# Kernel optimization log

Measured on AMD Instinct MI355X. Metric: run time of the kernel, lower is better.

## Reference

```python
import jax, jax.numpy as jnp
import numpy as np
import math

H = 16          # num_heads
EPS = 1e-5      # LayerNorm eps (torch default)


def setup_inputs() -> dict:
    key = jax.random.key(0)
    ks = jax.random.split(key, 4)
    B, T, D = 2, 2048, 1024
    s = 1.0 / math.sqrt(D)
    return {
        "x": jax.random.normal(ks[0], (B, T, D), dtype=jnp.float32),
        "ln_g": jnp.ones((D,), jnp.float32),
        "ln_b": jnp.zeros((D,), jnp.float32),
        "Wq": jax.random.normal(ks[1], (D, D), jnp.float32) * s,
        "bq": jnp.zeros((D,), jnp.float32),
        "Wk": jax.random.normal(ks[2], (D, D), jnp.float32) * s,
        "bk": jnp.zeros((D,), jnp.float32),
        "Wv": jax.random.normal(ks[3], (D, D), jnp.float32) * s,
        "bv": jnp.zeros((D,), jnp.float32),
    }


def reference(x, ln_g, ln_b, Wq, bq, Wk, bk, Wv, bv):
    B, T, D = x.shape
    # LayerNorm (shared across the three projections, computed once)
    mu = jnp.mean(x, axis=-1, keepdims=True)
    var = jnp.mean(jnp.square(x - mu), axis=-1, keepdims=True)
    xn = (x - mu) * jax.lax.rsqrt(var + EPS) * ln_g + ln_b
    # Q/K/V projections -> [B, T, H, Dh]
    q = (xn @ Wq + bq).reshape(B, T, H, D // H)
    k = (xn @ Wk + bk).reshape(B, T, H, D // H)
    v = (xn @ Wv + bv).reshape(B, T, H, D // H)
    # QK^T scores [B, n, m, h], scaled by sqrt(head_dim)
    scale = 1.0 / math.sqrt(D // H)
    attn = jnp.einsum('bnhd,bmhd->bnmh', q, k) * scale
    # softmax over key axis (dim=2), dropout p=0 is identity
    w = jax.nn.softmax(attn, axis=2)
    # weighted sum of values, merge heads
    y = jnp.einsum('bnmh,bmhd->bnhd', w, v).reshape(B, T, D)
    return y
```

## Files before the change

kernel.cpp:

```cpp
#include <hip/hip_runtime.h>
#include <hip/hip_bf16.h>


typedef __attribute__((ext_vector_type(8)))  short short8;
typedef __attribute__((ext_vector_type(4)))  float f32x4;
typedef __attribute__((ext_vector_type(2)))  float f32x2;
typedef __attribute__((ext_vector_type(16))) float f32x16;
typedef __attribute__((ext_vector_type(2)))  unsigned int uint2v;

#define D_MODEL 1024
#define T_SEQ   2048
#define NHEAD   16
#define HDIM    64

#define LOG2E 1.4426950408889634f

#if defined(__has_builtin)
#if __has_builtin(__builtin_amdgcn_exp2f)
#define EXP2(x) __builtin_amdgcn_exp2f(x)
#endif
#if __has_builtin(__builtin_amdgcn_permlane32_swap)
#define HAVE_PERMSWAP 1
#endif
#endif
#ifndef EXP2
#define EXP2(x) exp2f(x)
#endif

__device__ __forceinline__ unsigned short f2bf(float x) {
    unsigned int u = __float_as_uint(x);
    u = (u + 0x7fffu + ((u >> 16) & 1u)) >> 16;
    return (unsigned short)u;
}

__device__ __forceinline__ uint2v permswap(unsigned a, unsigned b) {
#ifdef HAVE_PERMSWAP
    return __builtin_amdgcn_permlane32_swap(a, b, false, false);
#else
    uint2v r;
    const unsigned as = (unsigned)__shfl_xor((int)a, 32, 64);
    const unsigned bs = (unsigned)__shfl_xor((int)b, 32, 64);
    const bool hi = (threadIdx.x & 32) != 0;
    r[0] = hi ? bs : a;
    r[1] = hi ? b  : as;
    return r;
#endif
}

__device__ __forceinline__ void w8(unsigned short* p, const uint4 v) {
    uint2 a; a.x = v.x; a.y = v.y;
    uint2 b; b.x = v.z; b.y = v.w;
    *(uint2*)p = a;
    *(uint2*)(p + 4) = b;
}

__device__ __forceinline__ short8 read8(const unsigned short* p) {
    union { unsigned u[4]; short8 s; } r;
    const uint2 a = *(const uint2*)p;
    const uint2 b = *(const uint2*)(p + 4);
    r.u[0] = a.x; r.u[1] = a.y; r.u[2] = b.x; r.u[3] = b.y;
    return r.s;
}

__global__ __launch_bounds__(256) void ln_wcast_kernel(
    const float* __restrict__ x, const float* __restrict__ gam,
    const float* __restrict__ bet, unsigned short* __restrict__ xn,
    const float* __restrict__ Wq, const float* __restrict__ Wk,
    const float* __restrict__ Wv, unsigned short* __restrict__ Wt)
{
    __shared__ float red[8];
    __shared__ float tile[32][33];
    const int bid = blockIdx.x;
    if (bid < 4096) {
        const int row = bid;
        const int t = threadIdx.x;
        const float4 v = ((const float4*)(x + (size_t)row * D_MODEL))[t];
        float s  = v.x + v.y + v.z + v.w;
        float s2 = v.x * v.x + v.y * v.y + v.z * v.z + v.w * v.w;
#pragma unroll
        for (int off = 32; off; off >>= 1) {
            s  += __shfl_down(s,  off, 64);
            s2 += __shfl_down(s2, off, 64);
        }
        const int lane = t & 63, wave = t >> 6;
        if (lane == 0) { red[wave] = s; red[4 + wave] = s2; }
        __syncthreads();
        s  = red[0] + red[1] + red[2] + red[3];
        s2 = red[4] + red[5] + red[6] + red[7];
        const float mu   = s * (1.f / D_MODEL);
        const float var  = s2 * (1.f / D_MODEL) - mu * mu;
        const float rstd = rsqrtf(var + 1e-5f);
        const float4 gv = ((const float4*)gam)[t];
        const float4 bv = ((const float4*)bet)[t];
        ushort4 o;
        o.x = f2bf((v.x - mu) * rstd * gv.x + bv.x);
        o.y = f2bf((v.y - mu) * rstd * gv.y + bv.y);
        o.z = f2bf((v.z - mu) * rstd * gv.z + bv.z);
        o.w = f2bf((v.w - mu) * rstd * gv.w + bv.w);
        ((ushort4*)(xn + (size_t)row * D_MODEL))[t] = o;
    } else {
        const int id = bid - 4096;
        const int z  = id >> 10;
        const int t2 = id & 1023;
        const int n0 = (t2 & 31) * 32, k0 = (t2 >> 5) * 32;
        const float* W = (z == 0) ? Wq : (z == 1) ? Wk : Wv;
        unsigned short* outw = Wt + (size_t)z * D_MODEL * D_MODEL;
        const int tx = threadIdx.x & 31, ty = threadIdx.x >> 5;
#pragma unroll
        for (int i = ty; i < 32; i += 8)
            tile[i][tx] = W[(size_t)(k0 + i) * D_MODEL + n0 + tx];
        __syncthreads();
#pragma unroll
        for (int i = ty; i < 32; i += 8)
            outw[(size_t)(n0 + i) * D_MODEL + k0 + tx] = f2bf(tile[tx][i]);
    }
}

__global__ __launch_bounds__(256) void qkv_gemm_kernel(
    const unsigned short* __restrict__ xn, const unsigned short* __restrict__ Wt,
    const float* __restrict__ bq, const float* __restrict__ bk, const float* __restrict__ bv,
    unsigned short* __restrict__ qo, unsigned short* __restrict__ ko, unsigned short* __restrict__ vt)
{
    const int which = blockIdx.x >> 3;
    const int xt = blockIdx.x & 7, yt = blockIdx.y;
    const bool vmode = (which == 2);
    const unsigned short* Aptr = vmode ? (Wt + (size_t)2 * D_MODEL * D_MODEL) : xn;
    const unsigned short* Bptr = vmode ? xn : (Wt + (size_t)which * D_MODEL * D_MODEL);
    const float* bias   = (which == 0) ? bq : (which == 1) ? bk : bv;
    const float scale   = (which == 0) ? (0.125f * LOG2E) : 1.0f;
    const int m0 = vmode ? (yt & 15) * 64 : yt * 64;
    const int n0 = vmode ? (xt + (yt >> 4) * 8) * 128 : xt * 128;

    __shared__ unsigned short As[64][64];
    __shared__ unsigned short Bs[128][64];

    const int tid = threadIdx.x;
    const int lane = tid & 63, wave = tid >> 6;
    const int wc = wave;
    const int g = lane >> 4, c = lane & 15;

    const int srow = lane >> 3;
    const int swzc = (((lane & 7) * 8) ^ ((srow & 7) * 8));
    const int rsw  = (c & 7) * 8;

    f32x4 acc[4][2] = {};

    for (int kt = 0; kt < D_MODEL; kt += 64) {
        __syncthreads();
#pragma unroll
        for (int i = 0; i < 2; ++i) {
            const int r = wave * 16 + i * 8;
            const unsigned short* ga = Aptr + (size_t)(m0 + r + srow) * D_MODEL + kt + swzc;
            __builtin_amdgcn_global_load_lds(
                (const __attribute__((address_space(1))) unsigned int*)ga,
                (__attribute__((address_space(3))) unsigned int*)(&As[r][0]), 16, 0, 0);
        }
#pragma unroll
        for (int i = 0; i < 4; ++i) {
            const int r = wave * 32 + i * 8;
            const unsigned short* gb = Bptr + (size_t)(n0 + r + srow) * D_MODEL + kt + swzc;
            __builtin_amdgcn_global_load_lds(
                (const __attribute__((address_space(1))) unsigned int*)gb,
                (__attribute__((address_space(3))) unsigned int*)(&Bs[r][0]), 16, 0, 0);
        }
        __syncthreads();

        short8 af[4][2], bf[2][2];
#pragma unroll
        for (int i = 0; i < 4; ++i) {
            const int ra = i * 16 + c;
#pragma unroll
            for (int kk = 0; kk < 2; ++kk)
                af[i][kk] = *(const short8*)(&As[ra][(kk * 32 + g * 8) ^ rsw]);
        }
#pragma unroll
        for (int j = 0; j < 2; ++j) {
            const int rb = wc * 32 + j * 16 + c;
#pragma unroll
            for (int kk = 0; kk < 2; ++kk)
                bf[j][kk] = *(const short8*)(&Bs[rb][(kk * 32 + g * 8) ^ rsw]);
        }
#pragma unroll
        for (int kk = 0; kk < 2; ++kk)
#pragma unroll
            for (int i = 0; i < 4; ++i)
#pragma unroll
                for (int j = 0; j < 2; ++j)
                    acc[i][j] = __builtin_amdgcn_mfma_f32_16x16x32_bf16(
                        af[i][kk], bf[j][kk], acc[i][j], 0, 0, 0);
    }

    if (!vmode) {
        unsigned short* out = (which == 0) ? qo : ko;
#pragma unroll
        for (int j = 0; j < 2; ++j) {
            const int n = n0 + wc * 32 + j * 16 + c;
            const float bn = bias[n];
            const int h = n >> 6, dh = n & 63;
#pragma unroll
            for (int i = 0; i < 4; ++i) {
#pragma unroll
                for (int r = 0; r < 4; ++r) {
                    const int m = m0 + i * 16 + g * 4 + r;
                    const int bb = m >> 11, t = m & 2047;
                    out[((size_t)(bb * NHEAD + h) * T_SEQ + t) * HDIM + dh] =
                        f2bf((acc[i][j][r] + bn) * scale);
                }
            }
        }
    } else {
#pragma unroll
        for (int i = 0; i < 4; ++i) {
#pragma unroll
            for (int r = 0; r < 4; ++r) {
                const int m = m0 + i * 16 + g * 4 + r;
                const float bn = bias[m];
#pragma unroll
                for (int j = 0; j < 2; ++j) {
                    const int n = n0 + wc * 32 + j * 16 + c;
                    const int bb = n >> 11, t = n & 2047;
                    vt[(size_t)bb * (D_MODEL * T_SEQ) + (size_t)m * T_SEQ + t] =
                        f2bf(acc[i][j][r] + bn);
                }
            }
        }
    }
}

__global__ __launch_bounds__(256, 4) void attn_kernel(
    const unsigned short* __restrict__ qb, const unsigned short* __restrict__ kb,
    const unsigned short* __restrict__ vtb, float* __restrict__ out)
{
    const int id  = blockIdx.x;
    const int swz = (id & 7) * 128 + (id >> 3);
    const int qt  = swz & 31;
    const int bh  = swz >> 5;
    const int b = bh >> 4, head = bh & 15;
    const unsigned short* Q  = qb  + (size_t)bh * T_SEQ * HDIM;
    const unsigned short* Kp = kb  + (size_t)bh * T_SEQ * HDIM;
    const unsigned short* Vt = vtb + (size_t)b * (D_MODEL * T_SEQ)
                                   + (size_t)head * (HDIM * T_SEQ);

    __shared__ __align__(16) unsigned short smem[17920];

    const int tid = threadIdx.x, lane = tid & 63, wave = tid >> 6;
    const int w2 = wave & 1, kvh = wave >> 1;
    const int q = lane & 31, h = lane >> 5;
    const int kvbase = kvh * (T_SEQ / 2);

    unsigned short* kbuf = &smem[wave * 4480];
    unsigned short* vbuf = kbuf + 2176;

    const int krow = lane >> 3, kch = (lane & 7) * 8;
    const int vrow = lane >> 2, vch = (lane & 3) * 8;

    short8 qf[4];
    {
        const unsigned short* qp = Q + (size_t)(qt * 64 + w2 * 32 + q) * HDIM;
#pragma unroll
        for (int c = 0; c < 4; ++c)
            qf[c] = *(const short8*)(qp + c * 16 + h * 8);
    }

    float l_r = 0.f;
    f32x16 o[2] = {};

    {
        const unsigned short* kp = Kp + (size_t)(kvbase + krow) * HDIM + kch;
        const unsigned short* vp = Vt + (size_t)vrow * T_SEQ + kvbase + vch;
        uint4 kr[4], vr[4];
#pragma unroll
        for (int i = 0; i < 4; ++i) kr[i] = *(const uint4*)(kp + (size_t)i * 8 * HDIM);
#pragma unroll
        for (int i = 0; i < 4; ++i) vr[i] = *(const uint4*)(vp + (size_t)i * 16 * T_SEQ);
#pragma unroll
        for (int i = 0; i < 4; ++i) w8(kbuf + (i * 8 + krow) * 68 + kch, kr[i]);
#pragma unroll
        for (int i = 0; i < 4; ++i) w8(vbuf + (i * 16 + vrow) * 36 + vch, vr[i]);
    }

#pragma unroll 1
    for (int t = 0; t < 32; ++t) {
        const bool more = (t + 1 < 32);
        const int kvn = kvbase + (t + 1) * 32;

        uint4 kr[4];
        if (more) {
            const unsigned short* kp = Kp + (size_t)(kvn + krow) * HDIM + kch;
#pragma unroll
            for (int i = 0; i < 4; ++i) kr[i] = *(const uint4*)(kp + (size_t)i * 8 * HDIM);
        }

        f32x16 s = {};
#pragma unroll
        for (int c = 0; c < 4; ++c) {
            const short8 kf = read8(kbuf + (size_t)q * 68 + c * 16 + h * 8);
            s = __builtin_amdgcn_mfma_f32_32x32x16_bf16(kf, qf[c], s, 0, 0, 0);
        }

#pragma unroll
        for (int r = 0; r < 16; ++r) { s[r] = EXP2(s[r]); }

        {
            f32x2 u[8];
#pragma unroll
            for (int r = 0; r < 8; ++r) { f32x2 a; a[0] = s[2*r]; a[1] = s[2*r+1]; u[r] = a; }
            u[0] += u[1]; u[2] += u[3]; u[4] += u[5]; u[6] += u[7];
            u[0] += u[2]; u[4] += u[6];
            u[0] += u[4];
            float rs = u[0][0] + u[0][1];
            rs += __shfl_xor(rs, 32, 64);
            l_r += rs;
        }

        unsigned Wb[8];
#pragma unroll
        for (int u = 0; u < 4; ++u) {
            asm("v_cvt_pk_bf16_f32 %0, %1, %2" : "=v"(Wb[u*2])   : "v"(s[4*u]),   "v"(s[4*u+1]));
            asm("v_cvt_pk_bf16_f32 %0, %1, %2" : "=v"(Wb[u*2+1]) : "v"(s[4*u+2]), "v"(s[4*u+3]));
        }

        short8 pf[2];
#pragma unroll
        for (int m = 0; m < 2; ++m) {
            const uint2v r0 = permswap(Wb[4*m],     Wb[4*m + 2]);
            const uint2v r1 = permswap(Wb[4*m + 1], Wb[4*m + 3]);
            union { unsigned u[4]; short8 s; } pw;
            pw.u[0] = r0[0]; pw.u[1] = r1[0]; pw.u[2] = r0[1]; pw.u[3] = r1[1];
            pf[m] = pw.s;
        }

        if (more) {
#pragma unroll
            for (int i = 0; i < 4; ++i) w8(kbuf + (i * 8 + krow) * 68 + kch, kr[i]);
        }
        uint4 vr[4];
        if (more) {
            const unsigned short* vp = Vt + (size_t)vrow * T_SEQ + kvn + vch;
#pragma unroll
            for (int i = 0; i < 4; ++i) vr[i] = *(const uint4*)(vp + (size_t)i * 16 * T_SEQ);
        }

#pragma unroll
        for (int dt = 0; dt < 2; ++dt) {
#pragma unroll
            for (int kk = 0; kk < 2; ++kk) {
                const short8 vf = read8(vbuf + (size_t)(dt * 32 + q) * 36 + kk * 16 + h * 8);
                o[dt] = __builtin_amdgcn_mfma_f32_32x32x16_bf16(vf, pf[kk], o[dt], 0, 0, 0);
            }
        }

        if (more) {
#pragma unroll
            for (int i = 0; i < 4; ++i) w8(vbuf + (i * 16 + vrow) * 36 + vch, vr[i]);
        }
    }

    __syncthreads();
    float* obuf  = (float*)(void*)smem;
    float* l_lds = ((float*)(void*)smem) + 64 * 68;

    const int qrl = w2 * 32 + q;
    if (kvh == 0) {
#pragma unroll
        for (int dt = 0; dt < 2; ++dt)
#pragma unroll
            for (int u = 0; u < 4; ++u) {
                float* dst = obuf + (size_t)qrl * 68 + dt * 32 + 8 * u + 4 * h;
                float2 lo; lo.x = o[dt][4*u];     lo.y = o[dt][4*u + 1];
                float2 hi; hi.x = o[dt][4*u + 2]; hi.y = o[dt][4*u + 3];
                *(float2*)dst = lo;
                *(float2*)(dst + 2) = hi;
            }
        if (h == 0) l_lds[qrl] = l_r;
    }
    __syncthreads();
    if (kvh == 1) {
        const float invl = 1.0f / (l_lds[qrl] + l_r);
#pragma unroll
        for (int dt = 0; dt < 2; ++dt)
#pragma unroll
            for (int u = 0; u < 4; ++u) {
                float* dst = obuf + (size_t)qrl * 68 + dt * 32 + 8 * u + 4 * h;
                float2 lo = *(const float2*)dst;
                float2 hi = *(const float2*)(dst + 2);
                lo.x = (lo.x + o[dt][4*u])     * invl;
                lo.y = (lo.y + o[dt][4*u + 1]) * invl;
                hi.x = (hi.x + o[dt][4*u + 2]) * invl;
                hi.y = (hi.y + o[dt][4*u + 3]) * invl;
                *(float2*)dst = lo;
                *(float2*)(dst + 2) = hi;
            }
    }
    __syncthreads();
#pragma unroll
    for (int it = 0; it < 2; ++it) {
        const int row = it * 32 + (tid >> 3);
        const int col = (tid & 7) * 8;
        const float4 v0 = *(const float4*)(&obuf[(size_t)row * 68 + col]);
        const float4 v1 = *(const float4*)(&obuf[(size_t)row * 68 + col + 4]);
        float* op = &out[(size_t)(b * T_SEQ + qt * 64 + row) * D_MODEL + head * HDIM + col];
        *(float4*)op = v0;
        *(float4*)(op + 4) = v1;
    }
}

extern "C" void kernel_launch(void* const* d_in, const int* in_sizes, int n_in,
                              void* d_out, int out_size, void* d_ws, size_t ws_size,
                              hipStream_t stream)
{
    const float* x   = (const float*)d_in[0];
    const float* lng = (const float*)d_in[1];
    const float* lnb = (const float*)d_in[2];
    const float* Wq  = (const float*)d_in[3];
    const float* bq  = (const float*)d_in[4];
    const float* Wk  = (const float*)d_in[5];
    const float* bk  = (const float*)d_in[6];
    const float* Wv  = (const float*)d_in[7];
    const float* bv  = (const float*)d_in[8];
    float* out = (float*)d_out;

    unsigned short* xn = (unsigned short*)d_ws;
    unsigned short* Wt = xn + (size_t)4096 * 1024;
    unsigned short* qh = Wt + (size_t)3 * 1024 * 1024;
    unsigned short* kh = qh + (size_t)4096 * 1024;
    unsigned short* vt = kh + (size_t)4096 * 1024;

    ln_wcast_kernel<<<7168, 256, 0, stream>>>(x, lng, lnb, xn, Wq, Wk, Wv, Wt);
    qkv_gemm_kernel<<<dim3(24, 64), 256, 0, stream>>>(xn, Wt, bq, bk, bv, qh, kh, vt);
    attn_kernel<<<1024, 256, 0, stream>>>(qh, kh, vt, out);
}
```

Before: 111.9 us.

## Share double-buffered K/V LDS tiles across wave pairs in attention and swizzle GEMM grid

The attention kernel now has each pair of waves that covers the same KV half load one shared K/V tile cooperatively. This halves the per-wave global loads and LDS writes. The tile is double-buffered in LDS, synchronized with a block barrier each iteration, and the MFMA sections are raised in priority with s_setprio. The V tile row pitch shrinks to 34 elements, which may break 8-byte alignment of the LDS accesses. Separately, the QKV GEMM launch becomes a 1D grid with a block swizzle for better cache locality, and the weight transpose-cast uses vectorized float4 loads and ushort4 stores.

```diff
diff --git a/kernel.cpp b/kernel.cpp
--- a/kernel.cpp
+++ b/kernel.cpp
@@ -45,6 +45,12 @@
     r[1] = hi ? b  : as;
     return r;
 #endif
+}
+
+__device__ __forceinline__ void group_barrier() {
+    asm volatile("s_waitcnt lgkmcnt(0)" ::: "memory");
+    __builtin_amdgcn_s_barrier();
+    asm volatile("" ::: "memory");
 }
 
 __device__ __forceinline__ void w8(unsigned short* p, const uint4 v) {
@@ -105,14 +111,19 @@
         const int n0 = (t2 & 31) * 32, k0 = (t2 >> 5) * 32;
         const float* W = (z == 0) ? Wq : (z == 1) ? Wk : Wv;
         unsigned short* outw = Wt + (size_t)z * D_MODEL * D_MODEL;
-        const int tx = threadIdx.x & 31, ty = threadIdx.x >> 5;
-#pragma unroll
-        for (int i = ty; i < 32; i += 8)
-            tile[i][tx] = W[(size_t)(k0 + i) * D_MODEL + n0 + tx];
+        const int lk = threadIdx.x >> 3;
+        const int ln = (threadIdx.x & 7) * 4;
+        *(float4*)&tile[lk][ln] =
+            *(const float4*)&W[(size_t)(k0 + lk) * D_MODEL + n0 + ln];
         __syncthreads();
-#pragma unroll
-        for (int i = ty; i < 32; i += 8)
-            outw[(size_t)(n0 + i) * D_MODEL + k0 + tx] = f2bf(tile[tx][i]);
+        const int wn = threadIdx.x >> 3;
+        const int wk = (threadIdx.x & 7) * 4;
+        ushort4 o4;
+        o4.x = f2bf(tile[wk + 0][wn]);
+        o4.y = f2bf(tile[wk + 1][wn]);
+        o4.z = f2bf(tile[wk + 2][wn]);
+        o4.w = f2bf(tile[wk + 3][wn]);
+        *(ushort4*)&outw[(size_t)(n0 + wn) * D_MODEL + k0 + wk] = o4;
     }
 }
 
@@ -121,8 +132,12 @@
     const float* __restrict__ bq, const float* __restrict__ bk, const float* __restrict__ bv,
     unsigned short* __restrict__ qo, unsigned short* __restrict__ ko, unsigned short* __restrict__ vt)
 {
-    const int which = blockIdx.x >> 3;
-    const int xt = blockIdx.x & 7, yt = blockIdx.y;
+    const int id  = blockIdx.x;
+    const int swz = (id & 7) * 192 + (id >> 3);
+    const int bx  = swz % 24;
+    const int yt  = swz / 24;
+    const int which = bx >> 3;
+    const int xt = bx & 7;
     const bool vmode = (which == 2);
     const unsigned short* Aptr = vmode ? (Wt + (size_t)2 * D_MODEL * D_MODEL) : xn;
     const unsigned short* Bptr = vmode ? xn : (Wt + (size_t)which * D_MODEL * D_MODEL);
@@ -241,22 +256,22 @@
     const unsigned short* Vt = vtb + (size_t)b * (D_MODEL * T_SEQ)
                                    + (size_t)head * (HDIM * T_SEQ);
 
-    __shared__ __align__(16) unsigned short smem[17920];
+    __shared__ __align__(16) unsigned short smem[17408];
 
     const int tid = threadIdx.x, lane = tid & 63, wave = tid >> 6;
-    const int w2 = wave & 1, kvh = wave >> 1;
+    const int grp = wave >> 1, qs = wave & 1;
     const int q = lane & 31, h = lane >> 5;
-    const int kvbase = kvh * (T_SEQ / 2);
-
-    unsigned short* kbuf = &smem[wave * 4480];
-    unsigned short* vbuf = kbuf + 2176;
-
-    const int krow = lane >> 3, kch = (lane & 7) * 8;
-    const int vrow = lane >> 2, vch = (lane & 3) * 8;
+    const int kvbase = grp * (T_SEQ / 2);
+
+    const int gtid = tid & 127;
+    const int krow = gtid >> 3, kcol = (gtid & 7) * 8;
+    const int vrow = gtid >> 2, vcol = (gtid & 3) * 8;
+
+    unsigned short* gbase = &smem[grp * 8704];
 
     short8 qf[4];
     {
-        const unsigned short* qp = Q + (size_t)(qt * 64 + w2 * 32 + q) * HDIM;
+        const unsigned short* qp = Q + (size_t)(qt * 64 + qs * 32 + q) * HDIM;
 #pragma unroll
         for (int c = 0; c < 4; ++c)
             qf[c] = *(const short8*)(qp + c * 16 + h * 8);
@@ -265,38 +280,43 @@
     float l_r = 0.f;
     f32x16 o[2] = {};
 
-    {
-        const unsigned short* kp = Kp + (size_t)(kvbase + krow) * HDIM + kch;
-        const unsigned short* vp = Vt + (size_t)vrow * T_SEQ + kvbase + vch;
-        uint4 kr[4], vr[4];
-#pragma unroll
-        for (int i = 0; i < 4; ++i) kr[i] = *(const uint4*)(kp + (size_t)i * 8 * HDIM);
-#pragma unroll
-        for (int i = 0; i < 4; ++i) vr[i] = *(const uint4*)(vp + (size_t)i * 16 * T_SEQ);
-#pragma unroll
-        for (int i = 0; i < 4; ++i) w8(kbuf + (i * 8 + krow) * 68 + kch, kr[i]);
-#pragma unroll
-        for (int i = 0; i < 4; ++i) w8(vbuf + (i * 16 + vrow) * 36 + vch, vr[i]);
-    }
-
+    const unsigned short* kp0 = Kp + (size_t)(kvbase + krow) * HDIM + kcol;
+    const unsigned short* vp0 = Vt + (size_t)vrow * T_SEQ + kvbase + vcol;
+    uint4 kr0 = *(const uint4*)(kp0);
+    uint4 kr1 = *(const uint4*)(kp0 + 16 * HDIM);
+    uint4 vr0 = *(const uint4*)(vp0);
+    uint4 vr1 = *(const uint4*)(vp0 + 32 * T_SEQ);
+    w8(gbase + krow * 68 + kcol, kr0);
+    w8(gbase + (krow + 16) * 68 + kcol, kr1);
+    w8(gbase + 4352 + vrow * 34 + vcol, vr0);
+    w8(gbase + 4352 + (vrow + 32) * 34 + vcol, vr1);
+    kp0 += 32 * HDIM;
+    vp0 += 32;
+
+    int cur = 0;
 #pragma unroll 1
     for (int t = 0; t < 32; ++t) {
         const bool more = (t + 1 < 32);
-        const int kvn = kvbase + (t + 1) * 32;
-
-        uint4 kr[4];
         if (more) {
-            const unsigned short* kp = Kp + (size_t)(kvn + krow) * HDIM + kch;
-#pragma unroll
-            for (int i = 0; i < 4; ++i) kr[i] = *(const uint4*)(kp + (size_t)i * 8 * HDIM);
-        }
+            kr0 = *(const uint4*)(kp0);
+            kr1 = *(const uint4*)(kp0 + 16 * HDIM);
+            vr0 = *(const uint4*)(vp0);
+            vr1 = *(const uint4*)(vp0 + 32 * T_SEQ);
+            kp0 += 32 * HDIM;
+            vp0 += 32;
+        }
+        group_barrier();
+        const unsigned short* kbuf = gbase + cur * 2176;
+        const unsigned short* vbuf = gbase + 4352 + cur * 2176;
 
         f32x16 s = {};
+        __builtin_amdgcn_s_setprio(1);
 #pragma unroll
         for (int c = 0; c < 4; ++c) {
             const short8 kf = read8(kbuf + (size_t)q * 68 + c * 16 + h * 8);
             s = __builtin_amdgcn_mfma_f32_32x32x16_bf16(kf, qf[c], s, 0, 0, 0);
         }
+        __builtin_amdgcn_s_setprio(0);
 
 #pragma unroll
         for (int r = 0; r < 16; ++r) { s[r] = EXP2(s[r]); }
@@ -330,38 +350,34 @@
             pf[m] = pw.s;
         }
 
-        if (more) {
-#pragma unroll
-            for (int i = 0; i < 4; ++i) w8(kbuf + (i * 8 + krow) * 68 + kch, kr[i]);
-        }
-        uint4 vr[4];
-        if (more) {
-            const unsigned short* vp = Vt + (size_t)vrow * T_SEQ + kvn + vch;
-#pragma unroll
-            for (int i = 0; i < 4; ++i) vr[i] = *(const uint4*)(vp + (size_t)i * 16 * T_SEQ);
-        }
-
+        __builtin_amdgcn_s_setprio(1);
 #pragma unroll
         for (int dt = 0; dt < 2; ++dt) {
 #pragma unroll
             for (int kk = 0; kk < 2; ++kk) {
-                const short8 vf = read8(vbuf + (size_t)(dt * 32 + q) * 36 + kk * 16 + h * 8);
+                const short8 vf = read8(vbuf + (size_t)(dt * 32 + q) * 34 + kk * 16 + h * 8);
                 o[dt] = __builtin_amdgcn_mfma_f32_32x32x16_bf16(vf, pf[kk], o[dt], 0, 0, 0);
             }
         }
+        __builtin_amdgcn_s_setprio(0);
 
         if (more) {
-#pragma unroll
-            for (int i = 0; i < 4; ++i) w8(vbuf + (i * 16 + vrow) * 36 + vch, vr[i]);
-        }
+            unsigned short* kd = gbase + (cur ^ 1) * 2176;
+            unsigned short* vd = gbase + 4352 + (cur ^ 1) * 2176;
+            w8(kd + krow * 68 + kcol, kr0);
+            w8(kd + (krow + 16) * 68 + kcol, kr1);
+            w8(vd + vrow * 34 + vcol, vr0);
+            w8(vd + (vrow + 32) * 34 + vcol, vr1);
+        }
+        cur ^= 1;
     }
 
     __syncthreads();
     float* obuf  = (float*)(void*)smem;
     float* l_lds = ((float*)(void*)smem) + 64 * 68;
 
-    const int qrl = w2 * 32 + q;
-    if (kvh == 0) {
+    const int qrl = qs * 32 + q;
+    if (grp == 0) {
 #pragma unroll
         for (int dt = 0; dt < 2; ++dt)
 #pragma unroll
@@ -375,7 +391,7 @@
         if (h == 0) l_lds[qrl] = l_r;
     }
     __syncthreads();
-    if (kvh == 1) {
+    if (grp == 1) {
         const float invl = 1.0f / (l_lds[qrl] + l_r);
 #pragma unroll
         for (int dt = 0; dt < 2; ++dt)
@@ -427,6 +443,6 @@
     unsigned short* vt = kh + (size_t)4096 * 1024;
 
     ln_wcast_kernel<<<7168, 256, 0, stream>>>(x, lng, lnb, xn, Wq, Wk, Wv, Wt);
-    qkv_gemm_kernel<<<dim3(24, 64), 256, 0, stream>>>(xn, Wt, bq, bk, bv, qh, kh, vt);
+    qkv_gemm_kernel<<<1536, 256, 0, stream>>>(xn, Wt, bq, bk, bv, qh, kh, vt);
     attn_kernel<<<1024, 256, 0, stream>>>(qh, kh, vt, out);
 }
```

Result: slower. 233.5 us (+108.8%).
